# Performance work log

Hardware: AMD Instinct MI355X
Metric: run time of the kernel (lower is better)

## Reference

```python
import jax, jax.numpy as jnp
import numpy as np

CUTOFF = 1.6  # short_range_cutoff from init_kwargs
E = 20_000_000
N_ATOMS = 100_000


def setup_inputs() -> dict:
    key = jax.random.key(0)
    k1, k2, k3 = jax.random.split(key, 3)
    Rij = jax.random.normal(k1, (E, 3), dtype=jnp.float32)
    idx_i = jax.random.randint(k2, (E,), 0, N_ATOMS, dtype=jnp.int32)
    idx_j = jax.random.randint(k3, (E,), 0, N_ATOMS, dtype=jnp.int32)
    return {"Rij": Rij, "idx_i": idx_i, "idx_j": idx_j}


def reference(Rij, idx_i, idx_j):
    """Faithful jit-compatible version of FilterShortRange.forward.

    torch.nonzero produces a dynamic-size index list; under jit we use the
    static-size equivalent jnp.nonzero(size=E, fill_value=0) and a validity
    mask: the first n_sr entries of the compacted outputs are exactly the
    short-range edges (same order as torch), padding beyond n_sr is zeroed
    (indices set to -1).
    """
    rij = jnp.linalg.norm(Rij, axis=-1)              # [E] per-edge distance
    mask = rij <= CUTOFF                             # [E] bool
    n_sr = jnp.sum(mask)                             # number of short-range edges
    (cidx,) = jnp.nonzero(mask, size=E, fill_value=0)  # stable compaction indices
    valid = jnpp_arange(E) < n_sr if False else (jnp.arange(E) < n_sr)  # [E]
    Rij_sr = jnp.where(valid[:, None], Rij[cidx], 0.0)   # [E,3], first n_sr rows valid
    idx_i_sr = jnp.where(valid, idx_i[cidx], -1)
    idx_j_sr = jnp.where(valid, idx_j[cidx], -1)
    # (Rij_lr, idx_i_lr, idx_j_lr, Rij, idx_i, idx_j, count)
    return (Rij, idx_i, idx_j, Rij_sr, idx_i_sr, idx_j_sr, n_sr)
```

## Files before the change

kernel.cpp:

```cpp
#include <hip/hip_runtime.h>

#define CUTOFF 1.6f
#define BLOCK 256
#define EPT 4
#define EPB (BLOCK * EPT)

typedef float f32x4 __attribute__((ext_vector_type(4)));

__global__ void __launch_bounds__(BLOCK) k1_count_copy(
    const float* __restrict__ Rij, float* __restrict__ outRij,
    int* __restrict__ counts, long E)
{
  long b = blockIdx.x;
  int t = threadIdx.x;
  long base = b * (long)EPB + (long)t * EPT;
  int cnt = 0;
  if (base < E) {
    const f32x4* rp4 = (const f32x4*)(Rij + base * 3);
    f32x4* op4 = (f32x4*)(outRij + base * 3);
    float rr[12];
#pragma unroll
    for (int q = 0; q < 3; ++q) {
      f32x4 v = rp4[q];
      op4[q] = v;
      rr[4 * q + 0] = v.x; rr[4 * q + 1] = v.y;
      rr[4 * q + 2] = v.z; rr[4 * q + 3] = v.w;
    }
#pragma unroll
    for (int k = 0; k < EPT; ++k) {
      float x = rr[3 * k], y = rr[3 * k + 1], z = rr[3 * k + 2];
      float s = sqrtf(x * x + y * y + z * z);
      cnt += (s <= CUTOFF) ? 1 : 0;
    }
  }
#pragma unroll
  for (int d = 32; d > 0; d >>= 1) cnt += __shfl_down(cnt, d, 64);
  __shared__ int ssum;
  if (t == 0) ssum = 0;
  __syncthreads();
  if ((t & 63) == 0) atomicAdd(&ssum, cnt);
  __syncthreads();
  if (t == 0) counts[b] = ssum;
}

__global__ void __launch_bounds__(1024) k2_scan(
    int* __restrict__ counts, int nb, int* __restrict__ nsr,
    float* __restrict__ out_nsr)
{
  int t = threadIdx.x;
  int C = (nb + 1023) >> 10;
  int start = t * C;
  int end = min(start + C, nb);
  int sum = 0;
  for (int i = start; i < end; ++i) sum += counts[i];
  int lane = t & 63, wid = t >> 6;
  int v = sum;
#pragma unroll
  for (int d = 1; d < 64; d <<= 1) {
    int n = __shfl_up(v, d, 64);
    if (lane >= d) v += n;
  }
  __shared__ int wsum[16];
  if (lane == 63) wsum[wid] = v;
  __syncthreads();
  int woff = 0;
  for (int w = 0; w < wid; ++w) woff += wsum[w];
  int run = woff + v - sum;
  for (int i = start; i < end; ++i) {
    int c = counts[i];
    counts[i] = run;
    run += c;
  }
  if (t == 1023) {
    nsr[0] = run;
    out_nsr[0] = (float)run;
  }
}

__device__ __forceinline__ void coop_copy(float* __restrict__ dst,
                                          const float* __restrict__ src,
                                          int len, int t)
{
  int h = (int)(((16u - (unsigned)((unsigned long long)dst & 15ull)) >> 2) & 3u);
  if (h > len) h = len;
  if (t < h) dst[t] = src[t];
  int n4 = (len - h) >> 2;
  f32x4* d4 = (f32x4*)(dst + h);
  for (int q = t; q < n4; q += BLOCK) {
    int s = h + 4 * q;
    f32x4 v = {src[s], src[s + 1], src[s + 2], src[s + 3]};
    d4[q] = v;
  }
  int done = h + 4 * n4;
  int rem = len - done;
  if (t < rem) dst[done + t] = src[done + t];
}

__device__ __forceinline__ void coop_fill(float* __restrict__ base, long lo,
                                          long hi, float val, int t)
{
  long len = hi - lo;
  if (len <= 0) return;
  float* p = base + lo;
  int h = (int)(((16u - (unsigned)((unsigned long long)p & 15ull)) >> 2) & 3u);
  if ((long)h > len) h = (int)len;
  if (t < h) p[t] = val;
  long n4 = (len - h) >> 2;
  f32x4* d4 = (f32x4*)(p + h);
  f32x4 v = {val, val, val, val};
  for (long q = t; q < n4; q += BLOCK) d4[q] = v;
  long done = h + 4 * n4;
  int rem = (int)(len - done);
  if (t < rem) p[done + t] = val;
}

__global__ void __launch_bounds__(BLOCK) k3_scatter_fill(
    const float* __restrict__ Rij, const int* __restrict__ idx_i,
    const int* __restrict__ idx_j, const int* __restrict__ offs,
    const int* __restrict__ nsr, float* __restrict__ out, long E, int nb)
{
  long b = blockIdx.x;
  int t = threadIdx.x;
  int lane = t & 63, wid = t >> 6;
  long base = b * (long)EPB + (long)t * EPT;
  long n = nsr[0];

  __shared__ float sR[3 * EPB];
  __shared__ float sI[EPB];
  __shared__ float sJ[EPB];
  __shared__ int wsum[BLOCK / 64];

  f32x4 r0 = {}, r1 = {}, r2 = {};
  int4 ia = {}, ja = {};
  if (base < E) {
    const f32x4* rp4 = (const f32x4*)(Rij + base * 3);
    r0 = rp4[0]; r1 = rp4[1]; r2 = rp4[2];
    ia = *(const int4*)(idx_i + base);
    ja = *(const int4*)(idx_j + base);
  }

  {
    long len = 3 * (E - n);
    long share = ((len + nb - 1) / nb + 3) & ~3L;
    long lo = 5 * E + 3 * n + b * share;
    long hi = lo + share;
    long cap = 8 * E;
    if (hi > cap) hi = cap;
    coop_fill(out, lo, hi, 0.0f, t);
  }
  {
    long len = E - n;
    long share = ((len + nb - 1) / nb + 3) & ~3L;
    long lo = 8 * E + n + b * share;
    long hi = lo + share;
    long cap = 9 * E;
    if (hi > cap) hi = cap;
    coop_fill(out, lo, hi, -1.0f, t);
  }
  {
    long len = E - n;
    long share = ((len + nb - 1) / nb + 3) & ~3L;
    long lo = 9 * E + n + b * share;
    long hi = lo + share;
    long cap = 10 * E;
    if (hi > cap) hi = cap;
    coop_fill(out, lo, hi, -1.0f, t);
  }

  float rr[12];
  int ii[EPT], jj[EPT];
  unsigned m = 0;
  int cnt = 0;
  if (base < E) {
    rr[0] = r0.x; rr[1] = r0.y; rr[2] = r0.z; rr[3] = r0.w;
    rr[4] = r1.x; rr[5] = r1.y; rr[6] = r1.z; rr[7] = r1.w;
    rr[8] = r2.x; rr[9] = r2.y; rr[10] = r2.z; rr[11] = r2.w;
    ii[0] = ia.x; ii[1] = ia.y; ii[2] = ia.z; ii[3] = ia.w;
    jj[0] = ja.x; jj[1] = ja.y; jj[2] = ja.z; jj[3] = ja.w;
    f32x4 fi0 = {(float)ii[0], (float)ii[1], (float)ii[2], (float)ii[3]};
    f32x4 fj0 = {(float)jj[0], (float)jj[1], (float)jj[2], (float)jj[3]};
    *(f32x4*)(out + 3 * E + base) = fi0;
    *(f32x4*)(out + 4 * E + base) = fj0;
#pragma unroll
    for (int k = 0; k < EPT; ++k) {
      float x = rr[3 * k], y = rr[3 * k + 1], z = rr[3 * k + 2];
      float s = sqrtf(x * x + y * y + z * z);
      if (s <= CUTOFF) { m |= 1u << k; ++cnt; }
    }
  }

  int sv = cnt;
#pragma unroll
  for (int d = 1; d < 64; d <<= 1) {
    int nn = __shfl_up(sv, d, 64);
    if (lane >= d) sv += nn;
  }
  if (lane == 63) wsum[wid] = sv;
  __syncthreads();
  int woff = 0, bsum = 0;
#pragma unroll
  for (int w = 0; w < BLOCK / 64; ++w) {
    int s = wsum[w];
    if (w < wid) woff += s;
    bsum += s;
  }
  int texcl = woff + sv - cnt;

  if (base < E && m) {
    int p = texcl;
#pragma unroll
    for (int k = 0; k < EPT; ++k) {
      if (m & (1u << k)) {
        sR[3 * p + 0] = rr[3 * k + 0];
        sR[3 * p + 1] = rr[3 * k + 1];
        sR[3 * p + 2] = rr[3 * k + 2];
        sI[p] = (float)ii[k];
        sJ[p] = (float)jj[k];
        ++p;
      }
    }
  }
  __syncthreads();

  long off = offs[b];
  coop_copy(out + 5 * E + 3 * off, sR, 3 * bsum, t);
  coop_copy(out + 8 * E + off, sI, bsum, t);
  coop_copy(out + 9 * E + off, sJ, bsum, t);
}

extern "C" void kernel_launch(void* const* d_in, const int* in_sizes, int n_in,
                              void* d_out, int out_size, void* d_ws,
                              size_t ws_size, hipStream_t stream)
{
  const float* Rij = (const float*)d_in[0];
  const int* idx_i = (const int*)d_in[1];
  const int* idx_j = (const int*)d_in[2];
  long E = (long)in_sizes[1];
  float* out = (float*)d_out;

  int nb = (int)((E + EPB - 1) / EPB);
  int* counts = (int*)d_ws;
  int* nsr = counts + nb;

  k1_count_copy<<<nb, BLOCK, 0, stream>>>(Rij, out, counts, E);
  k2_scan<<<1, 1024, 0, stream>>>(counts, nb, nsr, out + 10 * E);
  k3_scatter_fill<<<nb, BLOCK, 0, stream>>>(Rij, idx_i, idx_j, counts, nsr,
                                            out, E, nb);
}
```

Measured before the change: 309.3 us.

## Drop single-block scan kernel; compute per-block offsets redundantly in scatter kernel

Removes the one-block scan launch between the count and scatter kernels. Each scatter block now reads all per-block counts and reduces them with a packed 64-bit sum that yields both its exclusive prefix offset and the total short-range count. The padding fills move after the compacted copy because they depend on that total. This saves a kernel launch and a serial scan step, but every block now rereads the whole counts array, which adds a large amount of redundant L2 traffic and ALU work.

```diff
diff --git a/kernel.cpp b/kernel.cpp
--- a/kernel.cpp
+++ b/kernel.cpp
@@ -41,40 +41,6 @@
   if ((t & 63) == 0) atomicAdd(&ssum, cnt);
   __syncthreads();
   if (t == 0) counts[b] = ssum;
-}
-
-__global__ void __launch_bounds__(1024) k2_scan(
-    int* __restrict__ counts, int nb, int* __restrict__ nsr,
-    float* __restrict__ out_nsr)
-{
-  int t = threadIdx.x;
-  int C = (nb + 1023) >> 10;
-  int start = t * C;
-  int end = min(start + C, nb);
-  int sum = 0;
-  for (int i = start; i < end; ++i) sum += counts[i];
-  int lane = t & 63, wid = t >> 6;
-  int v = sum;
-#pragma unroll
-  for (int d = 1; d < 64; d <<= 1) {
-    int n = __shfl_up(v, d, 64);
-    if (lane >= d) v += n;
-  }
-  __shared__ int wsum[16];
-  if (lane == 63) wsum[wid] = v;
-  __syncthreads();
-  int woff = 0;
-  for (int w = 0; w < wid; ++w) woff += wsum[w];
-  int run = woff + v - sum;
-  for (int i = start; i < end; ++i) {
-    int c = counts[i];
-    counts[i] = run;
-    run += c;
-  }
-  if (t == 1023) {
-    nsr[0] = run;
-    out_nsr[0] = (float)run;
-  }
 }
 
 __device__ __forceinline__ void coop_copy(float* __restrict__ dst,
@@ -114,21 +80,21 @@
   if (t < rem) p[done + t] = val;
 }
 
-__global__ void __launch_bounds__(BLOCK) k3_scatter_fill(
+__global__ void __launch_bounds__(BLOCK) k3_all(
     const float* __restrict__ Rij, const int* __restrict__ idx_i,
-    const int* __restrict__ idx_j, const int* __restrict__ offs,
-    const int* __restrict__ nsr, float* __restrict__ out, long E, int nb)
+    const int* __restrict__ idx_j, const int* __restrict__ counts,
+    float* __restrict__ out, long E, int nb)
 {
   long b = blockIdx.x;
   int t = threadIdx.x;
   int lane = t & 63, wid = t >> 6;
   long base = b * (long)EPB + (long)t * EPT;
-  long n = nsr[0];
 
   __shared__ float sR[3 * EPB];
   __shared__ float sI[EPB];
   __shared__ float sJ[EPB];
   __shared__ int wsum[BLOCK / 64];
+  __shared__ unsigned long long wpt[BLOCK / 64];
 
   f32x4 r0 = {}, r1 = {}, r2 = {};
   int4 ia = {}, ja = {};
@@ -139,33 +105,21 @@
     ja = *(const int4*)(idx_j + base);
   }
 
-  {
-    long len = 3 * (E - n);
-    long share = ((len + nb - 1) / nb + 3) & ~3L;
-    long lo = 5 * E + 3 * n + b * share;
-    long hi = lo + share;
-    long cap = 8 * E;
-    if (hi > cap) hi = cap;
-    coop_fill(out, lo, hi, 0.0f, t);
-  }
-  {
-    long len = E - n;
-    long share = ((len + nb - 1) / nb + 3) & ~3L;
-    long lo = 8 * E + n + b * share;
-    long hi = lo + share;
-    long cap = 9 * E;
-    if (hi > cap) hi = cap;
-    coop_fill(out, lo, hi, -1.0f, t);
-  }
-  {
-    long len = E - n;
-    long share = ((len + nb - 1) / nb + 3) & ~3L;
-    long lo = 9 * E + n + b * share;
-    long hi = lo + share;
-    long cap = 10 * E;
-    if (hi > cap) hi = cap;
-    coop_fill(out, lo, hi, -1.0f, t);
-  }
+  unsigned long long pt = 0;
+  for (int i = t; i < nb; i += BLOCK) {
+    unsigned c = (unsigned)counts[i];
+    pt += ((unsigned long long)c << 32) | (i < (int)b ? c : 0u);
+  }
+#pragma unroll
+  for (int d = 32; d > 0; d >>= 1) pt += __shfl_down(pt, d, 64);
+  if (lane == 0) wpt[wid] = pt;
+  __syncthreads();
+  unsigned long long ptot = 0;
+#pragma unroll
+  for (int w = 0; w < BLOCK / 64; ++w) ptot += wpt[w];
+  long off = (long)(unsigned)(ptot & 0xFFFFFFFFull);
+  long n = (long)(unsigned)(ptot >> 32);
+  if (b == 0 && t == 0) out[10 * E] = (float)n;
 
   float rr[12];
   int ii[EPT], jj[EPT];
@@ -222,10 +176,37 @@
   }
   __syncthreads();
 
-  long off = offs[b];
   coop_copy(out + 5 * E + 3 * off, sR, 3 * bsum, t);
   coop_copy(out + 8 * E + off, sI, bsum, t);
   coop_copy(out + 9 * E + off, sJ, bsum, t);
+
+  {
+    long len = 3 * (E - n);
+    long share = ((len + nb - 1) / nb + 3) & ~3L;
+    long lo = 5 * E + 3 * n + b * share;
+    long hi = lo + share;
+    long cap = 8 * E;
+    if (hi > cap) hi = cap;
+    coop_fill(out, lo, hi, 0.0f, t);
+  }
+  {
+    long len = E - n;
+    long share = ((len + nb - 1) / nb + 3) & ~3L;
+    long lo = 8 * E + n + b * share;
+    long hi = lo + share;
+    long cap = 9 * E;
+    if (hi > cap) hi = cap;
+    coop_fill(out, lo, hi, -1.0f, t);
+  }
+  {
+    long len = E - n;
+    long share = ((len + nb - 1) / nb + 3) & ~3L;
+    long lo = 9 * E + n + b * share;
+    long hi = lo + share;
+    long cap = 10 * E;
+    if (hi > cap) hi = cap;
+    coop_fill(out, lo, hi, -1.0f, t);
+  }
 }
 
 extern "C" void kernel_launch(void* const* d_in, const int* in_sizes, int n_in,
@@ -240,10 +221,7 @@
 
   int nb = (int)((E + EPB - 1) / EPB);
   int* counts = (int*)d_ws;
-  int* nsr = counts + nb;
 
   k1_count_copy<<<nb, BLOCK, 0, stream>>>(Rij, out, counts, E);
-  k2_scan<<<1, 1024, 0, stream>>>(counts, nb, nsr, out + 10 * E);
-  k3_scatter_fill<<<nb, BLOCK, 0, stream>>>(Rij, idx_i, idx_j, counts, nsr,
-                                            out, E, nb);
-}
+  k3_all<<<nb, BLOCK, 0, stream>>>(Rij, idx_i, idx_j, counts, out, E, nb);
+}
```

Result: slower. 445.8 us (+44.1%).
